# Kernel tuning notes

Hardware: AMD Instinct MI355X
Metric: run time of the kernel (lower is better)

Reference implementation:

```python
import jax, jax.numpy as jnp
import numpy as np

EMBED = 1024
HEADS = 16
HEAD_DIM = EMBED // HEADS
HIDDEN = 4 * EMBED
EPS = 1e-5


def layer_norm(x, g, b):
    mu = jnp.mean(x, axis=-1, keepdims=True)
    var = jnp.var(x, axis=-1, keepdims=True)
    return (x - mu) * jax.lax.rsqrt(var + EPS) * g + b


def setup_inputs() -> dict:
    key = jax.random.key(0)
    ks = jax.random.split(key, 12)
    s_e = 1.0 / np.sqrt(EMBED)
    s_h = 1.0 / np.sqrt(HIDDEN)
    return {
        "x": jax.random.normal(ks[0], (8, 1024, EMBED), dtype=jnp.float32),
        "ln1_g": jnp.ones((EMBED,), jnp.float32),
        "ln1_b": jnp.zeros((EMBED,), jnp.float32),
        "w_qkv": jax.random.normal(ks[1], (EMBED, 3 * EMBED), jnp.float32) * s_e,
        "b_qkv": jax.random.normal(ks[2], (3 * EMBED,), jnp.float32) * s_e,
        "w_out": jax.random.normal(ks[3], (EMBED, EMBED), jnp.float32) * s_e,
        "b_out": jax.random.normal(ks[4], (EMBED,), jnp.float32) * s_e,
        "ln2_g": jnp.ones((EMBED,), jnp.float32),
        "ln2_b": jnp.zeros((EMBED,), jnp.float32),
        "w_up": jax.random.normal(ks[5], (EMBED, HIDDEN), jnp.float32) * s_e,
        "b_up": jax.random.normal(ks[6], (HIDDEN,), jnp.float32) * s_e,
        "w_down": jax.random.normal(ks[7], (HIDDEN, EMBED), jnp.float32) * s_h,
        "b_down": jax.random.normal(ks[8], (EMBED,), jnp.float32) * s_h,
    }


def reference(x, ln1_g, ln1_b, w_qkv, b_qkv, w_out, b_out,
              ln2_g, ln2_b, w_up, b_up, w_down, b_down):
    B, T, C = x.shape
    # --- attention sub-block ---
    h = layer_norm(x, ln1_g, ln1_b)
    qkv = h @ w_qkv + b_qkv                                   # [B,T,3C]
    q, k, v = jnp.split(qkv, 3, axis=-1)
    def heads(t):  # [B,T,C] -> [B,H,T,D]
        return t.reshape(B, T, HEADS, HEAD_DIM).transpose(0, 2, 1, 3)
    q, k, v = heads(q), heads(k), heads(v)
    scale = HEAD_DIM ** -0.5
    attn = jax.nn.softmax(jnp.einsum('bhqd,bhkd->bhqk', q, k) * scale, axis=-1)
    y = jnp.einsum('bhqk,bhkd->bhqd', attn, v)                # [B,H,T,D]
    y = y.transpose(0, 2, 1, 3).reshape(B, T, C)
    x = x + y @ w_out + b_out
    # --- MLP sub-block ---
    h = layer_norm(x, ln2_g, ln2_b)
    h = jax.nn.relu(h @ w_up + b_up)
    x = x + h @ w_down + b_down
    return x
```

## Files before the change

### kernel.cpp

```cpp
#include <hip/hip_runtime.h>
#include <stdint.h>


typedef __attribute__((ext_vector_type(8))) short short8;
typedef __attribute__((ext_vector_type(4))) short short4v;
typedef __attribute__((ext_vector_type(4))) float floatx4;

#define NROWS 8192

__device__ __forceinline__ unsigned short f2bf(float f) {
    union { float f; unsigned u; } x; x.f = f;
    unsigned r = x.u + 0x7fffu + ((x.u >> 16) & 1u);
    return (unsigned short)(r >> 16);
}
__device__ __forceinline__ float bf2f(unsigned short h) {
    union { unsigned u; float f; } x; x.u = (unsigned)h << 16; return x.f;
}

__device__ __forceinline__ void gl2lds16(const unsigned short* g, unsigned short* l) {
    __builtin_amdgcn_global_load_lds(
        (const __attribute__((address_space(1))) unsigned int*)(uintptr_t)g,
        (__attribute__((address_space(3))) unsigned int*)(unsigned int)(uintptr_t)l,
        16, 0, 0);
}

__global__ __launch_bounds__(256) void prep_kernel(
    const float* __restrict__ w_qkv, const float* __restrict__ w_out,
    const float* __restrict__ w_up, const float* __restrict__ w_down,
    unsigned short* __restrict__ wqkvT, unsigned short* __restrict__ woutT,
    unsigned short* __restrict__ wupT, unsigned short* __restrict__ wdownT,
    const float* __restrict__ x, const float* __restrict__ g,
    const float* __restrict__ b, unsigned short* __restrict__ h1)
{
    int bid = blockIdx.x;
    __shared__ unsigned short tile[32][33];
    __shared__ float rs[4], rs2[4];
    if (bid < 12288) {
        const float* in; unsigned short* out; int K, N, nb, tb;
        if (bid < 3072)      { in = w_qkv;  out = wqkvT;  K = 1024; N = 3072; nb = 96;  tb = bid; }
        else if (bid < 4096) { in = w_out;  out = woutT;  K = 1024; N = 1024; nb = 32;  tb = bid - 3072; }
        else if (bid < 8192) { in = w_up;   out = wupT;   K = 1024; N = 4096; nb = 128; tb = bid - 4096; }
        else                 { in = w_down; out = wdownT; K = 4096; N = 1024; nb = 32;  tb = bid - 8192; }
        int n0 = (tb % nb) * 32, k0 = (tb / nb) * 32;
        int tx = threadIdx.x & 31, ty = threadIdx.x >> 5;
        #pragma unroll
        for (int i = 0; i < 4; ++i)
            tile[ty + i * 8][tx] = f2bf(in[(size_t)(k0 + ty + i * 8) * N + n0 + tx]);
        __syncthreads();
        #pragma unroll
        for (int i = 0; i < 4; ++i)
            out[(size_t)(n0 + ty + i * 8) * K + k0 + tx] = tile[tx][ty + i * 8];
    } else {
        int row = bid - 12288, t = threadIdx.x;
        const float4* xr = (const float4*)(x + (size_t)row * 1024);
        float4 v = xr[t];
        float s  = v.x + v.y + v.z + v.w;
        float s2 = v.x * v.x + v.y * v.y + v.z * v.z + v.w * v.w;
        #pragma unroll
        for (int off = 32; off; off >>= 1) {
            s  += __shfl_xor(s,  off, 64);
            s2 += __shfl_xor(s2, off, 64);
        }
        int w = t >> 6;
        if ((t & 63) == 0) { rs[w] = s; rs2[w] = s2; }
        __syncthreads();
        s  = rs[0] + rs[1] + rs[2] + rs[3];
        s2 = rs2[0] + rs2[1] + rs2[2] + rs2[3];
        float mean = s * (1.0f / 1024.0f);
        float var  = s2 * (1.0f / 1024.0f) - mean * mean;
        float rstd = rsqrtf(var + 1e-5f);
        float4 gv = ((const float4*)g)[t];
        float4 bv = ((const float4*)b)[t];
        ushort4 o;
        o.x = f2bf((v.x - mean) * rstd * gv.x + bv.x);
        o.y = f2bf((v.y - mean) * rstd * gv.y + bv.y);
        o.z = f2bf((v.z - mean) * rstd * gv.z + bv.z);
        o.w = f2bf((v.w - mean) * rstd * gv.w + bv.w);
        ((ushort4*)(h1 + (size_t)row * 1024))[t] = o;
    }
}

__global__ __launch_bounds__(256) void ln_bf16b(
    const unsigned short* __restrict__ x, const float* __restrict__ g,
    const float* __restrict__ b, unsigned short* __restrict__ out)
{
    int row = blockIdx.x, t = threadIdx.x;
    ushort4 hv = ((const ushort4*)(x + (size_t)row * 1024))[t];
    float v0 = bf2f(hv.x), v1 = bf2f(hv.y), v2 = bf2f(hv.z), v3 = bf2f(hv.w);
    float s  = v0 + v1 + v2 + v3;
    float s2 = v0 * v0 + v1 * v1 + v2 * v2 + v3 * v3;
    #pragma unroll
    for (int off = 32; off; off >>= 1) {
        s  += __shfl_xor(s,  off, 64);
        s2 += __shfl_xor(s2, off, 64);
    }
    __shared__ float rs[4], rs2[4];
    int w = t >> 6;
    if ((t & 63) == 0) { rs[w] = s; rs2[w] = s2; }
    __syncthreads();
    s  = rs[0] + rs[1] + rs[2] + rs[3];
    s2 = rs2[0] + rs2[1] + rs2[2] + rs2[3];
    float mean = s * (1.0f / 1024.0f);
    float var  = s2 * (1.0f / 1024.0f) - mean * mean;
    float rstd = rsqrtf(var + 1e-5f);
    float4 gv = ((const float4*)g)[t];
    float4 bv = ((const float4*)b)[t];
    ushort4 o;
    o.x = f2bf((v0 - mean) * rstd * gv.x + bv.x);
    o.y = f2bf((v1 - mean) * rstd * gv.y + bv.y);
    o.z = f2bf((v2 - mean) * rstd * gv.z + bv.z);
    o.w = f2bf((v3 - mean) * rstd * gv.w + bv.w);
    ((ushort4*)(out + (size_t)row * 1024))[t] = o;
}

template <int MODE>
__global__ __launch_bounds__(512, 2) void gemm_8ph(
    const unsigned short* __restrict__ A, const unsigned short* __restrict__ Bt,
    int M, int N, int K,
    const float* __restrict__ bias,
    unsigned short* __restrict__ outB)
{
    int m0 = blockIdx.x * 256, n0 = blockIdx.y * 256;
    int tid = threadIdx.x;
    int w = tid >> 6, l = tid & 63, quad = l >> 4, lr = l & 15;
    int wm = w >> 2, wn = w & 3;

    __shared__ unsigned short As[2][256 * 64];
    __shared__ unsigned short Bs[2][256 * 64];

    floatx4 acc[8][4];
    #pragma unroll
    for (int i = 0; i < 8; ++i)
        #pragma unroll
        for (int j = 0; j < 4; ++j)
            acc[i][j] = (floatx4){0.f, 0.f, 0.f, 0.f};

    int srow = l >> 3;
    int swz  = ((l & 7) ^ srow) * 8;
    int arow1 = (w < 4) ? 16 * w : 128 + 16 * (w - 4);
    const unsigned short* Ag = A  + (size_t)(m0 + arow1 + srow) * K + swz;
    const unsigned short* Bg = Bt + (size_t)(n0 + 16 * w + srow) * K + swz;
    int nt = K >> 6;

    auto SB = [&](unsigned short* dst, int h, int kt) {
        #pragma unroll
        for (int u = 0; u < 2; ++u)
            gl2lds16(Bg + (size_t)(128 * h + 8 * u) * K + kt * 64,
                     &dst[(128 * h + 16 * w + 8 * u) * 64]);
    };
    auto SA1 = [&](unsigned short* dst, int kt) {
        #pragma unroll
        for (int u = 0; u < 2; ++u)
            gl2lds16(Ag + (size_t)(8 * u) * K + kt * 64,
                     &dst[(arow1 + 8 * u) * 64]);
    };
    auto SA2 = [&](unsigned short* dst, int kt) {
        #pragma unroll
        for (int u = 0; u < 2; ++u)
            gl2lds16(Ag + (size_t)(64 + 8 * u) * K + kt * 64,
                     &dst[(arow1 + 64 + 8 * u) * 64]);
    };

    SB(Bs[0], 0, 0); SB(Bs[0], 1, 0); SA1(As[0], 0); SA2(As[0], 0);
    SB(Bs[1], 0, 1); SB(Bs[1], 1, 1); SA1(As[1], 1);
    asm volatile("s_waitcnt vmcnt(6)" ::: "memory");
    __builtin_amdgcn_s_barrier();

    for (int t = 0; t < nt; ++t) {
        int b = t & 1;
        const unsigned short* Asb = As[b];
        const unsigned short* Bsb = Bs[b];
        short8 bfr[4][2];
        #pragma unroll
        for (int p = 0; p < 4; ++p) {
            if (p == 0)      { if (t + 1 < nt) SA2(As[b ^ 1], t + 1); }
            else if (p == 1) { if (t + 2 < nt) SB(Bs[b], 0, t + 2); }
            else if (p == 2) { if (t + 2 < nt) SB(Bs[b], 1, t + 2); }
            else             { if (t + 2 < nt) SA1(As[b], t + 2); }

            if (p == 0) {
                #pragma unroll
                for (int j = 0; j < 4; ++j)
                    #pragma unroll
                    for (int s = 0; s < 2; ++s)
                        bfr[j][s] = *(const short8*)
                            &Bsb[(64 * wn + 16 * j + lr) * 64 +
                                 (((s * 4 + quad) ^ (lr & 7)) * 8)];
            }
            short8 af[2][2];
            #pragma unroll
            for (int i = 0; i < 2; ++i)
                #pragma unroll
                for (int s = 0; s < 2; ++s)
                    af[i][s] = *(const short8*)
                        &Asb[(128 * wm + 32 * p + 16 * i + lr) * 64 +
                             (((s * 4 + quad) ^ (lr & 7)) * 8)];

            __builtin_amdgcn_s_barrier();
            asm volatile("s_waitcnt lgkmcnt(0)" ::: "memory");
            __builtin_amdgcn_s_setprio(1);
            #pragma unroll
            for (int i = 0; i < 2; ++i)
                #pragma unroll
                for (int j = 0; j < 4; ++j) {
                    acc[2 * p + i][j] = __builtin_amdgcn_mfma_f32_16x16x32_bf16(
                        af[i][0], bfr[j][0], acc[2 * p + i][j], 0, 0, 0);
                    acc[2 * p + i][j] = __builtin_amdgcn_mfma_f32_16x16x32_bf16(
                        af[i][1], bfr[j][1], acc[2 * p + i][j], 0, 0, 0);
                }
            __builtin_amdgcn_s_setprio(0);
            if (p == 3) {
                if (t + 2 >= nt) asm volatile("s_waitcnt vmcnt(0)" ::: "memory");
                else             asm volatile("s_waitcnt vmcnt(6)" ::: "memory");
            }
            __builtin_amdgcn_s_barrier();
        }
    }

    #pragma unroll
    for (int mi = 0; mi < 8; ++mi)
        #pragma unroll
        for (int j = 0; j < 4; ++j)
            #pragma unroll
            for (int r = 0; r < 4; ++r) {
                int m = m0 + 128 * wm + 16 * mi + quad * 4 + r;
                int n = n0 + 64 * wn + 16 * j + lr;
                outB[(size_t)m * N + n] = f2bf(fmaxf(acc[mi][j][r] + bias[n], 0.f));
            }
}

template <int MODE>
__global__ __launch_bounds__(512, 2) void gemm_bn128(
    const unsigned short* __restrict__ A, const unsigned short* __restrict__ Bt,
    int M, int N, int K,
    const float* __restrict__ bias,
    const float* __restrict__ residF, const unsigned short* __restrict__ residB,
    float* __restrict__ outF, unsigned short* __restrict__ outB,
    unsigned short* __restrict__ qO, unsigned short* __restrict__ kO,
    unsigned short* __restrict__ vO)
{
    int m0 = blockIdx.x * 256, n0 = blockIdx.y * 128;
    int tid = threadIdx.x;
    int w = tid >> 6, l = tid & 63, quad = l >> 4, lr = l & 15;
    int wm = w >> 1, wn = w & 1;

    __shared__ unsigned short As[3][256 * 64];
    __shared__ unsigned short Bs[3][128 * 64];

    floatx4 acc[4][4];
    #pragma unroll
    for (int i = 0; i < 4; ++i)
        #pragma unroll
        for (int j = 0; j < 4; ++j)
            acc[i][j] = (floatx4){0.f, 0.f, 0.f, 0.f};

    int srow = l >> 3;
    int swz  = ((l & 7) ^ srow) * 8;
    const unsigned short* Ag = A  + (size_t)(m0 + 16 * w + srow) * K + swz;
    const unsigned short* Bg = Bt + (size_t)(n0 + 16 * w + srow) * K + swz;
    int nt = K >> 6;

    auto ST = [&](int buf, int kt) {
        #pragma unroll
        for (int u = 0; u < 2; ++u)
            gl2lds16(Ag + (size_t)(8 * u) * K + kt * 64,
                     &As[buf][(16 * w + 8 * u) * 64]);
        #pragma unroll
        for (int u = 0; u < 2; ++u)
            gl2lds16(Ag + (size_t)(128 + 8 * u) * K + kt * 64,
                     &As[buf][(128 + 16 * w + 8 * u) * 64]);
        #pragma unroll
        for (int u = 0; u < 2; ++u)
            gl2lds16(Bg + (size_t)(8 * u) * K + kt * 64,
                     &Bs[buf][(16 * w + 8 * u) * 64]);
    };

    ST(0, 0);
    if (nt > 1) ST(1, 1);
    asm volatile("s_waitcnt vmcnt(6)" ::: "memory");
    __builtin_amdgcn_s_barrier();

    int cur = 0, pre = 2;
    for (int t = 0; t < nt; ++t) {
        if (t + 2 < nt) ST(pre, t + 2);

        const unsigned short* Asb = As[cur];
        const unsigned short* Bsb = Bs[cur];
        short8 bfr[4][2], af[4][2];
        #pragma unroll
        for (int j = 0; j < 4; ++j)
            #pragma unroll
            for (int s = 0; s < 2; ++s)
                bfr[j][s] = *(const short8*)
                    &Bsb[(64 * wn + 16 * j + lr) * 64 +
                         (((s * 4 + quad) ^ (lr & 7)) * 8)];
        #pragma unroll
        for (int i = 0; i < 4; ++i)
            #pragma unroll
            for (int s = 0; s < 2; ++s)
                af[i][s] = *(const short8*)
                    &Asb[(64 * wm + 16 * i + lr) * 64 +
                         (((s * 4 + quad) ^ (lr & 7)) * 8)];

        #pragma unroll
        for (int i = 0; i < 4; ++i)
            #pragma unroll
            for (int j = 0; j < 4; ++j) {
                acc[i][j] = __builtin_amdgcn_mfma_f32_16x16x32_bf16(
                    af[i][0], bfr[j][0], acc[i][j], 0, 0, 0);
                acc[i][j] = __builtin_amdgcn_mfma_f32_16x16x32_bf16(
                    af[i][1], bfr[j][1], acc[i][j], 0, 0, 0);
            }

        if (t + 2 >= nt) asm volatile("s_waitcnt vmcnt(0)" ::: "memory");
        else             asm volatile("s_waitcnt vmcnt(6)" ::: "memory");
        __builtin_amdgcn_s_barrier();
        cur = (cur == 2) ? 0 : cur + 1;
        pre = (pre == 2) ? 0 : pre + 1;
    }

    if (MODE == 0) {
        int sel = (n0 + 64 * wn) >> 10;
        if (sel < 2) {
            const float qscale = (sel == 0) ? 0.125f : 1.0f;
            unsigned short* dst = (sel == 0) ? qO : kO;
            #pragma unroll
            for (int mi = 0; mi < 4; ++mi)
                #pragma unroll
                for (int j = 0; j < 4; ++j)
                    #pragma unroll
                    for (int r = 0; r < 4; ++r) {
                        int m = m0 + 64 * wm + 16 * mi + quad * 4 + r;
                        int n = n0 + 64 * wn + 16 * j + lr;
                        float c = (acc[mi][j][r] + bias[n]) * qscale;
                        int bb = m >> 10, tt = m & 1023;
                        int cc = n & 1023, hh = cc >> 6, d = cc & 63;
                        dst[(((size_t)(bb * 16 + hh)) * 1024 + tt) * 64 + d] = f2bf(c);
                    }
        } else {
            int bb = m0 >> 10;
            #pragma unroll
            for (int mi = 0; mi < 4; ++mi) {
                int t0 = (m0 & 1023) + 64 * wm + 16 * mi + quad * 4;
                #pragma unroll
                for (int j = 0; j < 4; ++j) {
                    int n = n0 + 64 * wn + 16 * j + lr;
                    int cc = n & 1023, hh = cc >> 6, d = cc & 63;
                    float bn = bias[n];
                    ushort4 pk;
                    pk.x = f2bf(acc[mi][j][0] + bn);
                    pk.y = f2bf(acc[mi][j][1] + bn);
                    pk.z = f2bf(acc[mi][j][2] + bn);
                    pk.w = f2bf(acc[mi][j][3] + bn);
                    *(ushort4*)&vO[((size_t)(bb * 16 + hh) * 64 + d) * 1024 + t0] = pk;
                }
            }
        }
    } else {
        #pragma unroll
        for (int mi = 0; mi < 4; ++mi)
            #pragma unroll
            for (int j = 0; j < 4; ++j)
                #pragma unroll
                for (int r = 0; r < 4; ++r) {
                    int m = m0 + 64 * wm + 16 * mi + quad * 4 + r;
                    int n = n0 + 64 * wn + 16 * j + lr;
                    float c = acc[mi][j][r] + bias[n];
                    if (MODE == 1)
                        outB[(size_t)m * N + n] = f2bf(c + residF[(size_t)m * N + n]);
                    else
                        outF[(size_t)m * N + n] = c + bf2f(residB[(size_t)m * N + n]);
                }
    }
}

__global__ __launch_bounds__(256, 2) void attn_kernel(
    const unsigned short* __restrict__ qg, const unsigned short* __restrict__ kg,
    const unsigned short* __restrict__ vtg, unsigned short* __restrict__ y)
{
    int bid = blockIdx.x;
    int bh = bid & 127, qt = bid >> 7;
    int b = bh >> 4, h = bh & 15;
    int tid = threadIdx.x;
    int w = tid >> 6, l = tid & 63, quad = l >> 4, lr = l & 15;

    __shared__ unsigned short Qs[128 * 64];
    __shared__ unsigned short Ks[2][64 * 64];
    __shared__ unsigned short Vs[2][64 * 64];
    __shared__ unsigned short Ps[4][32 * 68];

    int srow = l >> 3;
    int scol = ((l & 7) ^ srow) * 8;

    {
        const unsigned short* qbase = qg + (size_t)bh * 65536 + (size_t)(qt * 128) * 64;
        #pragma unroll
        for (int u = 0; u < 4; ++u)
            gl2lds16(qbase + (size_t)(32 * w + 8 * u + srow) * 64 + scol,
                     &Qs[(32 * w + 8 * u) * 64]);
    }
    const unsigned short* kbase = kg  + (size_t)bh * 65536;
    const unsigned short* vbase = vtg + (size_t)bh * 65536;

    #pragma unroll
    for (int u = 0; u < 2; ++u) {
        gl2lds16(kbase + (size_t)(16 * w + 8 * u + srow) * 64 + scol,
                 &Ks[0][(16 * w + 8 * u) * 64]);
        gl2lds16(vbase + (size_t)(16 * w + 8 * u + srow) * 1024 + scol,
                 &Vs[0][(16 * w + 8 * u) * 64]);
    }
    __syncthreads();

    short8 af[2][2];
    #pragma unroll
    for (int i = 0; i < 2; ++i)
        #pragma unroll
        for (int s = 0; s < 2; ++s)
            af[i][s] = *(const short8*)
                &Qs[(32 * w + 16 * i + lr) * 64 + ((s * 4 + quad) ^ (lr & 7)) * 8];

    floatx4 o[2][4];
    float lsum[2][4];
    #pragma unroll
    for (int i = 0; i < 2; ++i)
        #pragma unroll
        for (int j = 0; j < 4; ++j) o[i][j] = (floatx4){0.f, 0.f, 0.f, 0.f};
    #pragma unroll
    for (int i = 0; i < 2; ++i)
        #pragma unroll
        for (int r = 0; r < 4; ++r) lsum[i][r] = 0.f;

    for (int kt = 0; kt < 16; ++kt) {
        int cur = kt & 1;
        if (kt + 1 < 16) {
            const unsigned short* kb = kbase + (size_t)((kt + 1) * 64) * 64;
            const unsigned short* vb = vbase + (size_t)((kt + 1) * 64);
            #pragma unroll
            for (int u = 0; u < 2; ++u) {
                gl2lds16(kb + (size_t)(16 * w + 8 * u + srow) * 64 + scol,
                         &Ks[cur ^ 1][(16 * w + 8 * u) * 64]);
                gl2lds16(vb + (size_t)(16 * w + 8 * u + srow) * 1024 + scol,
                         &Vs[cur ^ 1][(16 * w + 8 * u) * 64]);
            }
        }

        short8 kf[4][2];
        #pragma unroll
        for (int j = 0; j < 4; ++j)
            #pragma unroll
            for (int s = 0; s < 2; ++s)
                kf[j][s] = *(const short8*)
                    &Ks[cur][(16 * j + lr) * 64 + ((s * 4 + quad) ^ (lr & 7)) * 8];

        floatx4 s[2][4];
        #pragma unroll
        for (int i = 0; i < 2; ++i)
            #pragma unroll
            for (int j = 0; j < 4; ++j) {
                s[i][j] = (floatx4){0.f, 0.f, 0.f, 0.f};
                #pragma unroll
                for (int st = 0; st < 2; ++st)
                    s[i][j] = __builtin_amdgcn_mfma_f32_16x16x32_bf16(
                        af[i][st], kf[j][st], s[i][j], 0, 0, 0);
            }

        #pragma unroll
        for (int i = 0; i < 2; ++i)
            #pragma unroll
            for (int j = 0; j < 4; ++j)
                #pragma unroll
                for (int r = 0; r < 4; ++r) {
                    float p = __expf(s[i][j][r]);
                    lsum[i][r] += p;
                    Ps[w][(16 * i + quad * 4 + r) * 68 + 16 * j + lr] = f2bf(p);
                }

        asm volatile("s_waitcnt lgkmcnt(0)" ::: "memory");

        short8 vf[4][2];
        #pragma unroll
        for (int j = 0; j < 4; ++j)
            #pragma unroll
            for (int s = 0; s < 2; ++s)
                vf[j][s] = *(const short8*)
                    &Vs[cur][(16 * j + lr) * 64 + ((s * 4 + quad) ^ (lr & 7)) * 8];

        #pragma unroll
        for (int i = 0; i < 2; ++i)
            #pragma unroll
            for (int st = 0; st < 2; ++st) {
                short4v p0 = *(const short4v*)&Ps[w][(16 * i + lr) * 68 + st * 32 + quad * 8];
                short4v p1 = *(const short4v*)&Ps[w][(16 * i + lr) * 68 + st * 32 + quad * 8 + 4];
                short8 pf;
                #pragma unroll
                for (int e = 0; e < 4; ++e) { pf[e] = p0[e]; pf[e + 4] = p1[e]; }
                #pragma unroll
                for (int j = 0; j < 4; ++j)
                    o[i][j] = __builtin_amdgcn_mfma_f32_16x16x32_bf16(
                        pf, vf[j][st], o[i][j], 0, 0, 0);
            }
        __syncthreads();
    }

    #pragma unroll
    for (int off = 8; off; off >>= 1)
        #pragma unroll
        for (int i = 0; i < 2; ++i)
            #pragma unroll
            for (int r = 0; r < 4; ++r)
                lsum[i][r] += __shfl_xor(lsum[i][r], off, 64);
    float rinv[2][4];
    #pragma unroll
    for (int i = 0; i < 2; ++i)
        #pragma unroll
        for (int r = 0; r < 4; ++r) rinv[i][r] = 1.0f / lsum[i][r];

    #pragma unroll
    for (int i = 0; i < 2; ++i)
        #pragma unroll
        for (int j = 0; j < 4; ++j)
            #pragma unroll
            for (int r = 0; r < 4; ++r) {
                int trow = qt * 128 + 32 * w + 16 * i + quad * 4 + r;
                int col  = h * 64 + 16 * j + lr;
                y[((size_t)b * 1024 + trow) * 1024 + col] =
                    f2bf(o[i][j][r] * rinv[i][r]);
            }
}

extern "C" void kernel_launch(void* const* d_in, const int* in_sizes, int n_in,
                              void* d_out, int out_size, void* d_ws, size_t ws_size,
                              hipStream_t stream)
{
    const float* x      = (const float*)d_in[0];
    const float* ln1_g  = (const float*)d_in[1];
    const float* ln1_b  = (const float*)d_in[2];
    const float* w_qkv  = (const float*)d_in[3];
    const float* b_qkv  = (const float*)d_in[4];
    const float* w_out  = (const float*)d_in[5];
    const float* b_out  = (const float*)d_in[6];
    const float* ln2_g  = (const float*)d_in[7];
    const float* ln2_b  = (const float*)d_in[8];
    const float* w_up   = (const float*)d_in[9];
    const float* b_up   = (const float*)d_in[10];
    const float* w_down = (const float*)d_in[11];
    const float* b_down = (const float*)d_in[12];

    char* ws = (char*)d_ws;
    unsigned short* wqkvT  = (unsigned short*)(ws + 0);
    unsigned short* woutT  = (unsigned short*)(ws + 6291456);
    unsigned short* wupT   = (unsigned short*)(ws + 8388608);
    unsigned short* wdownT = (unsigned short*)(ws + 16777216);
    unsigned short* x2     = (unsigned short*)(ws + 25165824);
    unsigned short* h1     = (unsigned short*)(ws + 58720256);
    unsigned short* qb     = (unsigned short*)(ws + 75497472);
    unsigned short* kb     = (unsigned short*)(ws + 92274688);
    unsigned short* vtb    = (unsigned short*)(ws + 109051904);
    unsigned short* yb     = (unsigned short*)(ws + 125829120);
    unsigned short* a2     = (unsigned short*)(ws + 75497472);
    unsigned short* h2     = h1;

    prep_kernel<<<20480, 256, 0, stream>>>(
        w_qkv, w_out, w_up, w_down, wqkvT, woutT, wupT, wdownT,
        x, ln1_g, ln1_b, h1);

    gemm_bn128<0><<<dim3(NROWS / 256, 3072 / 128), 512, 0, stream>>>(
        h1, wqkvT, NROWS, 3072, 1024, b_qkv,
        nullptr, nullptr, nullptr, nullptr, qb, kb, vtb);

    attn_kernel<<<1024, 256, 0, stream>>>(qb, kb, vtb, yb);

    gemm_bn128<1><<<dim3(NROWS / 256, 1024 / 128), 512, 0, stream>>>(
        yb, woutT, NROWS, 1024, 1024, b_out,
        x, nullptr, nullptr, x2, nullptr, nullptr, nullptr);

    ln_bf16b<<<NROWS, 256, 0, stream>>>(x2, ln2_g, ln2_b, h2);

    gemm_8ph<2><<<dim3(NROWS / 256, 4096 / 256), 512, 0, stream>>>(
        h2, wupT, NROWS, 4096, 1024, b_up, a2);

    gemm_bn128<3><<<dim3(NROWS / 256, 1024 / 128), 512, 0, stream>>>(
        a2, wdownT, NROWS, 1024, 4096, b_down,
        nullptr, x2, (float*)d_out, nullptr, nullptr, nullptr, nullptr);
}
```

Measured before the change: 433.2 us.

## Replace GEMM kernels with unified 128x128 two-phase double-buffered kernel

Removes the 256x256 eight-phase up-projection GEMM and the 256x128 triple-buffered GEMM. All four projections now go through a single 128x128-tile, 256-thread kernel that splits each k-step into two phases, interleaving global-to-LDS loads with MFMA and using barriers and setprio. Smaller tiles give more blocks and less LDS per block, which should help occupancy and load balance. The cost is lower data reuse per tile, so each block does more global and LDS traffic per FLOP.

```diff
diff --git a/kernel.cpp b/kernel.cpp
--- a/kernel.cpp
+++ b/kernel.cpp
@@ -114,123 +114,7 @@
 }
 
 template <int MODE>
-__global__ __launch_bounds__(512, 2) void gemm_8ph(
-    const unsigned short* __restrict__ A, const unsigned short* __restrict__ Bt,
-    int M, int N, int K,
-    const float* __restrict__ bias,
-    unsigned short* __restrict__ outB)
-{
-    int m0 = blockIdx.x * 256, n0 = blockIdx.y * 256;
-    int tid = threadIdx.x;
-    int w = tid >> 6, l = tid & 63, quad = l >> 4, lr = l & 15;
-    int wm = w >> 2, wn = w & 3;
-
-    __shared__ unsigned short As[2][256 * 64];
-    __shared__ unsigned short Bs[2][256 * 64];
-
-    floatx4 acc[8][4];
-    #pragma unroll
-    for (int i = 0; i < 8; ++i)
-        #pragma unroll
-        for (int j = 0; j < 4; ++j)
-            acc[i][j] = (floatx4){0.f, 0.f, 0.f, 0.f};
-
-    int srow = l >> 3;
-    int swz  = ((l & 7) ^ srow) * 8;
-    int arow1 = (w < 4) ? 16 * w : 128 + 16 * (w - 4);
-    const unsigned short* Ag = A  + (size_t)(m0 + arow1 + srow) * K + swz;
-    const unsigned short* Bg = Bt + (size_t)(n0 + 16 * w + srow) * K + swz;
-    int nt = K >> 6;
-
-    auto SB = [&](unsigned short* dst, int h, int kt) {
-        #pragma unroll
-        for (int u = 0; u < 2; ++u)
-            gl2lds16(Bg + (size_t)(128 * h + 8 * u) * K + kt * 64,
-                     &dst[(128 * h + 16 * w + 8 * u) * 64]);
-    };
-    auto SA1 = [&](unsigned short* dst, int kt) {
-        #pragma unroll
-        for (int u = 0; u < 2; ++u)
-            gl2lds16(Ag + (size_t)(8 * u) * K + kt * 64,
-                     &dst[(arow1 + 8 * u) * 64]);
-    };
-    auto SA2 = [&](unsigned short* dst, int kt) {
-        #pragma unroll
-        for (int u = 0; u < 2; ++u)
-            gl2lds16(Ag + (size_t)(64 + 8 * u) * K + kt * 64,
-                     &dst[(arow1 + 64 + 8 * u) * 64]);
-    };
-
-    SB(Bs[0], 0, 0); SB(Bs[0], 1, 0); SA1(As[0], 0); SA2(As[0], 0);
-    SB(Bs[1], 0, 1); SB(Bs[1], 1, 1); SA1(As[1], 1);
-    asm volatile("s_waitcnt vmcnt(6)" ::: "memory");
-    __builtin_amdgcn_s_barrier();
-
-    for (int t = 0; t < nt; ++t) {
-        int b = t & 1;
-        const unsigned short* Asb = As[b];
-        const unsigned short* Bsb = Bs[b];
-        short8 bfr[4][2];
-        #pragma unroll
-        for (int p = 0; p < 4; ++p) {
-            if (p == 0)      { if (t + 1 < nt) SA2(As[b ^ 1], t + 1); }
-            else if (p == 1) { if (t + 2 < nt) SB(Bs[b], 0, t + 2); }
-            else if (p == 2) { if (t + 2 < nt) SB(Bs[b], 1, t + 2); }
-            else             { if (t + 2 < nt) SA1(As[b], t + 2); }
-
-            if (p == 0) {
-                #pragma unroll
-                for (int j = 0; j < 4; ++j)
-                    #pragma unroll
-                    for (int s = 0; s < 2; ++s)
-                        bfr[j][s] = *(const short8*)
-                            &Bsb[(64 * wn + 16 * j + lr) * 64 +
-                                 (((s * 4 + quad) ^ (lr & 7)) * 8)];
-            }
-            short8 af[2][2];
-            #pragma unroll
-            for (int i = 0; i < 2; ++i)
-                #pragma unroll
-                for (int s = 0; s < 2; ++s)
-                    af[i][s] = *(const short8*)
-                        &Asb[(128 * wm + 32 * p + 16 * i + lr) * 64 +
-                             (((s * 4 + quad) ^ (lr & 7)) * 8)];
-
-            __builtin_amdgcn_s_barrier();
-            asm volatile("s_waitcnt lgkmcnt(0)" ::: "memory");
-            __builtin_amdgcn_s_setprio(1);
-            #pragma unroll
-            for (int i = 0; i < 2; ++i)
-                #pragma unroll
-                for (int j = 0; j < 4; ++j) {
-                    acc[2 * p + i][j] = __builtin_amdgcn_mfma_f32_16x16x32_bf16(
-                        af[i][0], bfr[j][0], acc[2 * p + i][j], 0, 0, 0);
-                    acc[2 * p + i][j] = __builtin_amdgcn_mfma_f32_16x16x32_bf16(
-                        af[i][1], bfr[j][1], acc[2 * p + i][j], 0, 0, 0);
-                }
-            __builtin_amdgcn_s_setprio(0);
-            if (p == 3) {
-                if (t + 2 >= nt) asm volatile("s_waitcnt vmcnt(0)" ::: "memory");
-                else             asm volatile("s_waitcnt vmcnt(6)" ::: "memory");
-            }
-            __builtin_amdgcn_s_barrier();
-        }
-    }
-
-    #pragma unroll
-    for (int mi = 0; mi < 8; ++mi)
-        #pragma unroll
-        for (int j = 0; j < 4; ++j)
-            #pragma unroll
-            for (int r = 0; r < 4; ++r) {
-                int m = m0 + 128 * wm + 16 * mi + quad * 4 + r;
-                int n = n0 + 64 * wn + 16 * j + lr;
-                outB[(size_t)m * N + n] = f2bf(fmaxf(acc[mi][j][r] + bias[n], 0.f));
-            }
-}
-
-template <int MODE>
-__global__ __launch_bounds__(512, 2) void gemm_bn128(
+__global__ __launch_bounds__(256, 2) void gemm_2b(
     const unsigned short* __restrict__ A, const unsigned short* __restrict__ Bt,
     int M, int N, int K,
     const float* __restrict__ bias,
@@ -239,13 +123,13 @@
     unsigned short* __restrict__ qO, unsigned short* __restrict__ kO,
     unsigned short* __restrict__ vO)
 {
-    int m0 = blockIdx.x * 256, n0 = blockIdx.y * 128;
+    int m0 = blockIdx.x * 128, n0 = blockIdx.y * 128;
     int tid = threadIdx.x;
     int w = tid >> 6, l = tid & 63, quad = l >> 4, lr = l & 15;
     int wm = w >> 1, wn = w & 1;
 
-    __shared__ unsigned short As[3][256 * 64];
-    __shared__ unsigned short Bs[3][128 * 64];
+    __shared__ unsigned short As[2][128 * 64];
+    __shared__ unsigned short Bs[2][128 * 64];
 
     floatx4 acc[4][4];
     #pragma unroll
@@ -256,67 +140,75 @@
 
     int srow = l >> 3;
     int swz  = ((l & 7) ^ srow) * 8;
-    const unsigned short* Ag = A  + (size_t)(m0 + 16 * w + srow) * K + swz;
-    const unsigned short* Bg = Bt + (size_t)(n0 + 16 * w + srow) * K + swz;
+    const unsigned short* Ag = A  + (size_t)(m0 + 32 * w + srow) * K + swz;
+    const unsigned short* Bg = Bt + (size_t)(n0 + 32 * w + srow) * K + swz;
     int nt = K >> 6;
 
-    auto ST = [&](int buf, int kt) {
-        #pragma unroll
-        for (int u = 0; u < 2; ++u)
+    auto SA = [&](unsigned short* dst, int kt) {
+        #pragma unroll
+        for (int u = 0; u < 4; ++u)
             gl2lds16(Ag + (size_t)(8 * u) * K + kt * 64,
-                     &As[buf][(16 * w + 8 * u) * 64]);
-        #pragma unroll
-        for (int u = 0; u < 2; ++u)
-            gl2lds16(Ag + (size_t)(128 + 8 * u) * K + kt * 64,
-                     &As[buf][(128 + 16 * w + 8 * u) * 64]);
-        #pragma unroll
-        for (int u = 0; u < 2; ++u)
+                     &dst[(32 * w + 8 * u) * 64]);
+    };
+    auto SB = [&](unsigned short* dst, int kt) {
+        #pragma unroll
+        for (int u = 0; u < 4; ++u)
             gl2lds16(Bg + (size_t)(8 * u) * K + kt * 64,
-                     &Bs[buf][(16 * w + 8 * u) * 64]);
+                     &dst[(32 * w + 8 * u) * 64]);
     };
 
-    ST(0, 0);
-    if (nt > 1) ST(1, 1);
-    asm volatile("s_waitcnt vmcnt(6)" ::: "memory");
+    SB(Bs[0], 0); SA(As[0], 0);
+    if (nt > 1) SB(Bs[1], 1);
+    asm volatile("s_waitcnt vmcnt(4)" ::: "memory");
     __builtin_amdgcn_s_barrier();
 
-    int cur = 0, pre = 2;
     for (int t = 0; t < nt; ++t) {
-        if (t + 2 < nt) ST(pre, t + 2);
-
-        const unsigned short* Asb = As[cur];
-        const unsigned short* Bsb = Bs[cur];
-        short8 bfr[4][2], af[4][2];
-        #pragma unroll
-        for (int j = 0; j < 4; ++j)
-            #pragma unroll
-            for (int s = 0; s < 2; ++s)
-                bfr[j][s] = *(const short8*)
-                    &Bsb[(64 * wn + 16 * j + lr) * 64 +
-                         (((s * 4 + quad) ^ (lr & 7)) * 8)];
-        #pragma unroll
-        for (int i = 0; i < 4; ++i)
-            #pragma unroll
-            for (int s = 0; s < 2; ++s)
-                af[i][s] = *(const short8*)
-                    &Asb[(64 * wm + 16 * i + lr) * 64 +
-                         (((s * 4 + quad) ^ (lr & 7)) * 8)];
-
-        #pragma unroll
-        for (int i = 0; i < 4; ++i)
-            #pragma unroll
-            for (int j = 0; j < 4; ++j) {
-                acc[i][j] = __builtin_amdgcn_mfma_f32_16x16x32_bf16(
-                    af[i][0], bfr[j][0], acc[i][j], 0, 0, 0);
-                acc[i][j] = __builtin_amdgcn_mfma_f32_16x16x32_bf16(
-                    af[i][1], bfr[j][1], acc[i][j], 0, 0, 0);
-            }
-
-        if (t + 2 >= nt) asm volatile("s_waitcnt vmcnt(0)" ::: "memory");
-        else             asm volatile("s_waitcnt vmcnt(6)" ::: "memory");
-        __builtin_amdgcn_s_barrier();
-        cur = (cur == 2) ? 0 : cur + 1;
-        pre = (pre == 2) ? 0 : pre + 1;
+        int b = t & 1;
+        const unsigned short* Asb = As[b];
+        const unsigned short* Bsb = Bs[b];
+        short8 bfr[4][2];
+        #pragma unroll
+        for (int p = 0; p < 2; ++p) {
+            if (p == 0) { if (t + 1 < nt) SA(As[b ^ 1], t + 1); }
+            else        { if (t + 2 < nt) SB(Bs[b], t + 2); }
+
+            if (p == 0) {
+                #pragma unroll
+                for (int j = 0; j < 4; ++j)
+                    #pragma unroll
+                    for (int s = 0; s < 2; ++s)
+                        bfr[j][s] = *(const short8*)
+                            &Bsb[(64 * wn + 16 * j + lr) * 64 +
+                                 (((s * 4 + quad) ^ (lr & 7)) * 8)];
+            }
+            short8 af[2][2];
+            #pragma unroll
+            for (int i = 0; i < 2; ++i)
+                #pragma unroll
+                for (int s = 0; s < 2; ++s)
+                    af[i][s] = *(const short8*)
+                        &Asb[(64 * wm + 32 * p + 16 * i + lr) * 64 +
+                             (((s * 4 + quad) ^ (lr & 7)) * 8)];
+
+            __builtin_amdgcn_s_barrier();
+            asm volatile("s_waitcnt lgkmcnt(0)" ::: "memory");
+            __builtin_amdgcn_s_setprio(1);
+            #pragma unroll
+            for (int i = 0; i < 2; ++i)
+                #pragma unroll
+                for (int j = 0; j < 4; ++j) {
+                    acc[2 * p + i][j] = __builtin_amdgcn_mfma_f32_16x16x32_bf16(
+                        af[i][0], bfr[j][0], acc[2 * p + i][j], 0, 0, 0);
+                    acc[2 * p + i][j] = __builtin_amdgcn_mfma_f32_16x16x32_bf16(
+                        af[i][1], bfr[j][1], acc[2 * p + i][j], 0, 0, 0);
+                }
+            __builtin_amdgcn_s_setprio(0);
+            if (p == 1) {
+                if (t + 2 >= nt) asm volatile("s_waitcnt vmcnt(0)" ::: "memory");
+                else             asm volatile("s_waitcnt vmcnt(4)" ::: "memory");
+            }
+            __builtin_amdgcn_s_barrier();
+        }
     }
 
     if (MODE == 0) {
@@ -368,6 +260,8 @@
                     float c = acc[mi][j][r] + bias[n];
                     if (MODE == 1)
                         outB[(size_t)m * N + n] = f2bf(c + residF[(size_t)m * N + n]);
+                    else if (MODE == 2)
+                        outB[(size_t)m * N + n] = f2bf(fmaxf(c, 0.f));
                     else
                         outF[(size_t)m * N + n] = c + bf2f(residB[(size_t)m * N + n]);
                 }
@@ -564,22 +458,23 @@
         w_qkv, w_out, w_up, w_down, wqkvT, woutT, wupT, wdownT,
         x, ln1_g, ln1_b, h1);
 
-    gemm_bn128<0><<<dim3(NROWS / 256, 3072 / 128), 512, 0, stream>>>(
+    gemm_2b<0><<<dim3(NROWS / 128, 3072 / 128), 256, 0, stream>>>(
         h1, wqkvT, NROWS, 3072, 1024, b_qkv,
         nullptr, nullptr, nullptr, nullptr, qb, kb, vtb);
 
     attn_kernel<<<1024, 256, 0, stream>>>(qb, kb, vtb, yb);
 
-    gemm_bn128<1><<<dim3(NROWS / 256, 1024 / 128), 512, 0, stream>>>(
+    gemm_2b<1><<<dim3(NROWS / 128, 1024 / 128), 256, 0, stream>>>(
         yb, woutT, NROWS, 1024, 1024, b_out,
         x, nullptr, nullptr, x2, nullptr, nullptr, nullptr);
 
     ln_bf16b<<<NROWS, 256, 0, stream>>>(x2, ln2_g, ln2_b, h2);
 
-    gemm_8ph<2><<<dim3(NROWS / 256, 4096 / 256), 512, 0, stream>>>(
-        h2, wupT, NROWS, 4096, 1024, b_up, a2);
-
-    gemm_bn128<3><<<dim3(NROWS / 256, 1024 / 128), 512, 0, stream>>>(
+    gemm_2b<2><<<dim3(NROWS / 128, 4096 / 128), 256, 0, stream>>>(
+        h2, wupT, NROWS, 4096, 1024, b_up,
+        nullptr, nullptr, nullptr, a2, nullptr, nullptr, nullptr);
+
+    gemm_2b<3><<<dim3(NROWS / 128, 1024 / 128), 256, 0, stream>>>(
         a2, wdownT, NROWS, 1024, 4096, b_down,
         nullptr, x2, (float*)d_out, nullptr, nullptr, nullptr, nullptr);
 }
```

Result: no change. 435.0 us (+0.4%).
